# Kernel tuning notes

Measured on AMD Instinct MI355X. Metric: run time of the kernel, lower is better.

## Reference

```python
import jax, jax.numpy as jnp
import numpy as np

N = 100_000        # nodes
E = 800_000        # directed edges before symmetrization
IN_DIM = 18        # input_dim_wf + input_dim_vm
HID = 128
VM_NUM = 16        # each_vm_type_num * vm_types
B = 65536 // VM_NUM
NEG_SLOPE = 0.2    # PyG GATConv leaky_relu slope


def _gat_conv(h, src, dst, W, a_s, a_d, b, n):
    """PyG GATConv (heads=1, add_self_loops=True, dropout off)."""
    z = h @ W                                     # [n, C]
    loops = jnp.arange(n, dtype=src.dtype)
    s = jnp.concatenate([src, loops])
    d = jnp.concatenate([dst, loops])
    e_s = z @ a_s                                 # [n]
    e_d = z @ a_d
    alpha = jax.nn.leaky_relu(e_s[s] + e_d[d], NEG_SLOPE)   # [E']
    amax = jax.ops.segment_max(alpha, d, num_segments=n)    # stable softmax over incoming edges
    ex = jnp.exp(alpha - amax[d])
    denom = jax.ops.segment_sum(ex, d, num_segments=n)
    w = ex / denom[d]
    out = jax.ops.segment_sum(w[:, None] * z[s], d, num_segments=n)
    return out + b


def setup_inputs() -> dict:
    key = jax.random.key(0)
    ks = jax.random.split(key, 16)
    sc = 0.1
    inp = {
        'state_wf': jax.random.normal(ks[0], (N, IN_DIM), jnp.float32),
        'edge_index': jax.random.randint(ks[1], (2, E), 0, N, jnp.int32),
        'candidate_task_index': jax.random.randint(ks[2], (B * VM_NUM,), 0, N, jnp.int32),
        # GAT layer 0: 18 -> 128
        'W0': jax.random.normal(ks[3], (IN_DIM, HID), jnp.float32) * sc,
        'a_src0': jax.random.normal(ks[4], (HID,), jnp.float32) * sc,
        'a_dst0': jax.random.normal(ks[5], (HID,), jnp.float32) * sc,
        'b0': jnp.zeros((HID,), jnp.float32),
        # GAT layer 1: 128 -> 128
        'W1': jax.random.normal(ks[6], (HID, HID), jnp.float32) * sc,
        'a_src1': jax.random.normal(ks[7], (HID,), jnp.float32) * sc,
        'a_dst1': jax.random.normal(ks[8], (HID,), jnp.float32) * sc,
        'b1': jnp.zeros((HID,), jnp.float32),
        # actor MLP: Linear(128,128) + ReLU + Linear(128,1)
        'mW0': jax.random.normal(ks[9], (HID, HID), jnp.float32) * sc,
        'mb0': jnp.zeros((HID,), jnp.float32),
        'mW1': jax.random.normal(ks[10], (HID, 1), jnp.float32) * sc,
        'mb1': jnp.zeros((1,), jnp.float32),
    }
    return inp


def reference(state_wf, edge_index, candidate_task_index,
              W0, a_src0, a_dst0, b0, W1, a_src1, a_dst1, b1,
              mW0, mb0, mW1, mb1):
    # Actor.forward symmetrizes edges: cat(edge_index, edge_index.flip(0))
    src = jnp.concatenate([edge_index[0], edge_index[1]])
    dst = jnp.concatenate([edge_index[1], edge_index[0]])
    # GAT stack, F.elu after each conv (dropout=0)
    h = jax.nn.elu(_gat_conv(state_wf, src, dst, W0, a_src0, a_dst0, b0, N))
    h = jax.nn.elu(_gat_conv(h, src, dst, W1, a_src1, a_dst1, b1, N))
    # gather candidate tasks and score them
    cand = h[candidate_task_index].reshape(-1, VM_NUM, HID)       # [B, vm, H]
    scores = jax.nn.relu(cand @ mW0 + mb0) @ mW1 + mb1            # [B, vm, 1]
    pi = jax.nn.softmax(scores, axis=1)[..., 0]                   # softmax over dim=1
    return pi
```

## Files before the change

### kernel.cpp

```cpp
#include <hip/hip_runtime.h>
#include <hip/hip_bf16.h>
#include <math.h>
#include <stdint.h>

typedef __hip_bfloat16 bf16;
typedef __attribute__((ext_vector_type(8))) short s8v;
typedef __attribute__((ext_vector_type(4))) float f4v;

#define N_NODES 100000
#define HID 128
#define NEG 0.2f
#define NBUCK 256
#define BSHIFT 9
#define INDIM 18

__device__ __forceinline__ float b2f(bf16 x) { return __bfloat162float(x); }
__device__ __forceinline__ bf16 f2b(float x) { return __float2bfloat16(x); }
__device__ __forceinline__ float lo_bf(unsigned int u) {
    union { unsigned int i; float f; } c; c.i = u << 16; return c.f;
}
__device__ __forceinline__ float hi_bf(unsigned int u) {
    union { unsigned int i; float f; } c; c.i = u & 0xffff0000u; return c.f;
}
__device__ __forceinline__ short bfbits(float x) {
    union { bf16 b; short s; } u; u.b = f2b(x); return u.s;
}


__global__ void k_bhist(const int* __restrict__ ei, int E, int* __restrict__ bcnt) {
    __shared__ int h[NBUCK];
    int t = threadIdx.x;
    h[t] = 0;
    __syncthreads();
    int i = blockIdx.x * blockDim.x + t;
    int stride = gridDim.x * blockDim.x;
    for (; i < E; i += stride) {
        int u = ei[i], v = ei[E + i];
        atomicAdd(&h[v >> BSHIFT], 1);
        atomicAdd(&h[u >> BSHIFT], 1);
    }
    __syncthreads();
    if (h[t]) atomicAdd(&bcnt[t], h[t]);
}

__global__ void k_bscan(const int* __restrict__ bcnt, int* __restrict__ bbase,
                        int* __restrict__ bnext) {
    __shared__ int buf[2][NBUCK];
    int t = threadIdx.x;
    int v = bcnt[t];
    buf[0][t] = v;
    __syncthreads();
    int cur = 0;
    for (int off = 1; off < NBUCK; off <<= 1) {
        int x = buf[cur][t] + ((t >= off) ? buf[cur][t - off] : 0);
        buf[cur ^ 1][t] = x;
        cur ^= 1;
        __syncthreads();
    }
    int incl = buf[cur][t];
    int excl = incl - v;
    bbase[t] = excl;
    bnext[t] = excl;
    if (t == NBUCK - 1) bbase[NBUCK] = incl;
}

#define SCH 2048
#define SK 8
__global__ __launch_bounds__(256) void k_bscatter(const int* __restrict__ ei, int E,
                                                  int* __restrict__ bnext,
                                                  unsigned* __restrict__ pairs) {
    __shared__ int h[NBUCK], base[NBUCK], h2[NBUCK];
    int t = threadIdx.x;
    h[t] = 0; h2[t] = 0;
    __syncthreads();
    int b0 = blockIdx.x * SCH;
    int eu[SK], ev[SK];
#pragma unroll
    for (int k = 0; k < SK; k++) {
        int i = b0 + k * 256 + t;
        if (i < E) {
            int u = ei[i], v = ei[E + i];
            eu[k] = u; ev[k] = v;
            atomicAdd(&h[v >> BSHIFT], 1);
            atomicAdd(&h[u >> BSHIFT], 1);
        } else { eu[k] = -1; ev[k] = -1; }
    }
    __syncthreads();
    if (h[t] > 0) base[t] = atomicAdd(&bnext[t], h[t]);
    __syncthreads();
#pragma unroll
    for (int k = 0; k < SK; k++) {
        if (eu[k] >= 0) {
            unsigned u = (unsigned)eu[k], v = (unsigned)ev[k];
            int bv = v >> BSHIFT;
            pairs[base[bv] + atomicAdd(&h2[bv], 1)] = ((v & 511u) << 17) | u;
            int bu = u >> BSHIFT;
            pairs[base[bu] + atomicAdd(&h2[bu], 1)] = ((u & 511u) << 17) | v;
        }
    }
}

__global__ __launch_bounds__(256) void k_bbuild(const unsigned* __restrict__ pairs,
                                                const int* __restrict__ bbase,
                                                int* __restrict__ rowptr,
                                                int* __restrict__ col, int n) {
    __shared__ int deg[512];
    __shared__ int off[512];
    __shared__ int s2[2][256];
    int t = threadIdx.x;
    int b = blockIdx.x;
    int node0 = b << BSHIFT;
    deg[t] = 0; deg[t + 256] = 0;
    __syncthreads();
    int p0 = bbase[b], p1 = bbase[b + 1];
    for (int i = p0 + t; i < p1; i += 256) atomicAdd(&deg[pairs[i] >> 17], 1);
    __syncthreads();
    int a0 = deg[2 * t], a1 = deg[2 * t + 1];
    int s = a0 + a1;
    s2[0][t] = s;
    __syncthreads();
    int cur = 0;
    for (int o = 1; o < 256; o <<= 1) {
        int x = s2[cur][t] + ((t >= o) ? s2[cur][t - o] : 0);
        s2[cur ^ 1][t] = x;
        cur ^= 1;
        __syncthreads();
    }
    int excl = s2[cur][t] - s;
    off[2 * t] = excl;
    off[2 * t + 1] = excl + a0;
    __syncthreads();
    for (int j = t; j < 512; j += 256) {
        int node = node0 + j;
        if (node <= n) rowptr[node] = p0 + off[j];
    }
    deg[t] = 0; deg[t + 256] = 0;
    __syncthreads();
    for (int i = p0 + t; i < p1; i += 256) {
        unsigned pr = pairs[i];
        int d = pr >> 17;
        int ofs = atomicAdd(&deg[d], 1);
        col[p0 + off[d] + ofs] = (int)(pr & 0x1FFFFu);
    }
}


__device__ void pack128(const float* __restrict__ W, short* __restrict__ frag, int b) {
    int idx = b * 256 + threadIdx.x;
    int j = idx & 7;
    int lane = (idx >> 3) & 63;
    int cb = (idx >> 9) & 7;
    int kb = idx >> 12;
    int k = kb * 32 + (lane >> 4) * 8 + j;
    int c = cb * 16 + (lane & 15);
    float w = W[k * HID + c];
    bf16 hi = f2b(w);
    frag[idx] = bfbits(w);
    frag[16384 + idx] = bfbits(w - b2f(hi));
}

__global__ void k_packall(const float* __restrict__ W1, const float* __restrict__ mW0,
                          const float* __restrict__ W0, short* __restrict__ W1f,
                          short* __restrict__ mW0f, short* __restrict__ W0f) {
    int b = blockIdx.x;
    if (b < 64) { pack128(W1, W1f, b); return; }
    if (b < 128) { pack128(mW0, mW0f, b - 64); return; }
    int idx = (b - 128) * 256 + threadIdx.x;
    int var = idx >> 13;
    int r = idx & 8191;
    int j = r & 7;
    int lane = (r >> 3) & 63;
    int cb = (r >> 9) & 7;
    int kb = r >> 12;
    int kp = kb * 32 + (lane >> 4) * 8 + j;
    int c = cb * 16 + (lane & 15);
    short out = 0;
    if (kp < 2 * INDIM) {
        int src = (kp < INDIM) ? kp : kp - INDIM;
        float w = W0[src * HID + c];
        bf16 hi = f2b(w);
        bool want_hi = (kp < INDIM) ^ (var == 1);
        out = want_hi ? bfbits(w) : bfbits(w - b2f(hi));
    }
    W0f[var * 8192 + r] = out;
}


__global__ __launch_bounds__(256) void k_feat0m(const float* __restrict__ x,
                        const short* __restrict__ Wf,
                        const float* __restrict__ as_, const float* __restrict__ ad_,
                        bf16* __restrict__ z, float* __restrict__ es, float* __restrict__ ed,
                        int n) {
    __shared__ __align__(16) short ztile[4][16][136];
    int wv = threadIdx.x >> 6, lane = threadIdx.x & 63;
    int node0 = (blockIdx.x * 4 + wv) * 16;
    if (node0 >= n) return;
    int m = lane & 15, q = lane >> 4;
    const float* xr = x + (size_t)(node0 + m) * INDIM;
    s8v af0, af1;
#pragma unroll
    for (int j = 0; j < 8; j++) {
        int p0 = q * 8 + j;
        float v0 = 0.f;
        if (p0 < INDIM) v0 = xr[p0];
        else if (p0 < 2 * INDIM) v0 = xr[p0 - INDIM];
        short o0;
        if (p0 < INDIM) o0 = bfbits(v0);
        else o0 = bfbits(v0 - b2f(f2b(v0)));
        af0[j] = o0;
        int p1 = 32 + q * 8 + j;
        float v1 = (p1 < 2 * INDIM) ? xr[p1 - INDIM] : 0.f;
        af1[j] = bfbits(v1 - b2f(f2b(v1)));
    }
    f4v acc[8];
#pragma unroll
    for (int cb = 0; cb < 8; cb++) acc[cb] = (f4v){0.f, 0.f, 0.f, 0.f};
    const s8v* wf = (const s8v*)Wf;
#pragma unroll
    for (int cb = 0; cb < 8; cb++) {
        acc[cb] = __builtin_amdgcn_mfma_f32_16x16x32_bf16(af0, wf[cb * 64 + lane], acc[cb], 0, 0, 0);
        acc[cb] = __builtin_amdgcn_mfma_f32_16x16x32_bf16(af1, wf[(8 + cb) * 64 + lane], acc[cb], 0, 0, 0);
        acc[cb] = __builtin_amdgcn_mfma_f32_16x16x32_bf16(af0, wf[1024 + cb * 64 + lane], acc[cb], 0, 0, 0);
        acc[cb] = __builtin_amdgcn_mfma_f32_16x16x32_bf16(af1, wf[1024 + (8 + cb) * 64 + lane], acc[cb], 0, 0, 0);
    }
    float pe[4] = {0.f, 0.f, 0.f, 0.f}, pd[4] = {0.f, 0.f, 0.f, 0.f};
#pragma unroll
    for (int cb = 0; cb < 8; cb++) {
        float asv = as_[cb * 16 + m];
        float adv = ad_[cb * 16 + m];
#pragma unroll
        for (int r = 0; r < 4; r++) { pe[r] += acc[cb][r] * asv; pd[r] += acc[cb][r] * adv; }
    }
#pragma unroll
    for (int r = 0; r < 4; r++) {
#pragma unroll
        for (int off = 1; off < 16; off <<= 1) {
            pe[r] += __shfl_xor(pe[r], off);
            pd[r] += __shfl_xor(pd[r], off);
        }
    }
    if (m == 0) {
#pragma unroll
        for (int r = 0; r < 4; r++) {
            es[node0 + q * 4 + r] = pe[r];
            ed[node0 + q * 4 + r] = pd[r];
        }
    }
#pragma unroll
    for (int cb = 0; cb < 8; cb++)
#pragma unroll
        for (int r = 0; r < 4; r++)
            ztile[wv][q * 4 + r][cb * 16 + m] = bfbits(acc[cb][r]);
#pragma unroll
    for (int i = 0; i < 4; i++) {
        int idx = i * 64 + lane;
        int row = idx >> 4, t = idx & 15;
        s8v v = *(const s8v*)&ztile[wv][row][t * 8];
        *(s8v*)((short*)z + (size_t)(node0 + row) * HID + t * 8) = v;
    }
}


__global__ __launch_bounds__(256) void k_feat1(const bf16* __restrict__ h,
                        const short* __restrict__ Wf,
                        const float* __restrict__ as_, const float* __restrict__ ad_,
                        bf16* __restrict__ z, float* __restrict__ es, float* __restrict__ ed,
                        int n) {
    __shared__ __align__(16) short ztile[4][16][136];
    int wv = threadIdx.x >> 6, lane = threadIdx.x & 63;
    int node0 = (blockIdx.x * 4 + wv) * 16;
    if (node0 >= n) return;
    int m = lane & 15, q = lane >> 4;
    const short* hrow = (const short*)h + (size_t)(node0 + m) * HID + q * 8;
    s8v af[4];
#pragma unroll
    for (int kb = 0; kb < 4; kb++) af[kb] = *(const s8v*)(hrow + kb * 32);
    f4v acc[8];
#pragma unroll
    for (int cb = 0; cb < 8; cb++) acc[cb] = (f4v){0.f, 0.f, 0.f, 0.f};
    const s8v* wf = (const s8v*)Wf;
#pragma unroll
    for (int kb = 0; kb < 4; kb++) {
#pragma unroll
        for (int cb = 0; cb < 8; cb++) {
            acc[cb] = __builtin_amdgcn_mfma_f32_16x16x32_bf16(af[kb], wf[(kb * 8 + cb) * 64 + lane], acc[cb], 0, 0, 0);
            acc[cb] = __builtin_amdgcn_mfma_f32_16x16x32_bf16(af[kb], wf[2048 + (kb * 8 + cb) * 64 + lane], acc[cb], 0, 0, 0);
        }
    }
    float pe[4] = {0.f, 0.f, 0.f, 0.f}, pd[4] = {0.f, 0.f, 0.f, 0.f};
#pragma unroll
    for (int cb = 0; cb < 8; cb++) {
        float asv = as_[cb * 16 + m];
        float adv = ad_[cb * 16 + m];
#pragma unroll
        for (int r = 0; r < 4; r++) { pe[r] += acc[cb][r] * asv; pd[r] += acc[cb][r] * adv; }
    }
#pragma unroll
    for (int r = 0; r < 4; r++) {
#pragma unroll
        for (int off = 1; off < 16; off <<= 1) {
            pe[r] += __shfl_xor(pe[r], off);
            pd[r] += __shfl_xor(pd[r], off);
        }
    }
    if (m == 0) {
#pragma unroll
        for (int r = 0; r < 4; r++) {
            es[node0 + q * 4 + r] = pe[r];
            ed[node0 + q * 4 + r] = pd[r];
        }
    }
#pragma unroll
    for (int cb = 0; cb < 8; cb++)
#pragma unroll
        for (int r = 0; r < 4; r++)
            ztile[wv][q * 4 + r][cb * 16 + m] = bfbits(acc[cb][r]);
#pragma unroll
    for (int i = 0; i < 4; i++) {
        int idx = i * 64 + lane;
        int row = idx >> 4, t = idx & 15;
        s8v v = *(const s8v*)&ztile[wv][row][t * 8];
        *(s8v*)((short*)z + (size_t)(node0 + row) * HID + t * 8) = v;
    }
}


__global__ __launch_bounds__(256) void k_agg(const bf16* __restrict__ z,
                      const int* __restrict__ rowptr, const int* __restrict__ col,
                      const float* __restrict__ es, const float* __restrict__ ed,
                      const float* __restrict__ bias, bf16* __restrict__ hout, int n) {
    int wv = threadIdx.x >> 6;
    int lane = threadIdx.x & 63;
    int d = blockIdx.x * 4 + wv;
    if (d >= n) return;
    int s0 = rowptr[d], s1 = rowptr[d + 1];
    float edv = ed[d];
    int g = lane >> 4, t = lane & 15;
    const uint4* zr = (const uint4*)z;
    float acc[8];
#pragma unroll
    for (int j = 0; j < 8; j++) acc[j] = 0.f;
    float den = 0.f;
    for (int e0 = s0; e0 < s1; e0 += 8) {
        int eA = e0 + g, eB = e0 + 4 + g;
        bool okA = (eA < s1), okB = (eB < s1);
        int sA = col[okA ? eA : s1 - 1];
        int sB = col[okB ? eB : s1 - 1];
        float aA = es[sA] + edv; aA = aA > 0.f ? aA : NEG * aA;
        float aB = es[sB] + edv; aB = aB > 0.f ? aB : NEG * aB;
        float pA = okA ? __expf(fminf(aA, 15.f)) : 0.f;
        float pB = okB ? __expf(fminf(aB, 15.f)) : 0.f;
        uint4 rA = zr[(size_t)sA * 16 + t];
        uint4 rB = zr[(size_t)sB * 16 + t];
        den += pA + pB;
        acc[0] += pA * lo_bf(rA.x) + pB * lo_bf(rB.x);
        acc[1] += pA * hi_bf(rA.x) + pB * hi_bf(rB.x);
        acc[2] += pA * lo_bf(rA.y) + pB * lo_bf(rB.y);
        acc[3] += pA * hi_bf(rA.y) + pB * hi_bf(rB.y);
        acc[4] += pA * lo_bf(rA.z) + pB * lo_bf(rB.z);
        acc[5] += pA * hi_bf(rA.z) + pB * hi_bf(rB.z);
        acc[6] += pA * lo_bf(rA.w) + pB * lo_bf(rB.w);
        acc[7] += pA * hi_bf(rA.w) + pB * hi_bf(rB.w);
    }
#pragma unroll
    for (int off = 16; off <= 32; off <<= 1) {
        den += __shfl_xor(den, off);
#pragma unroll
        for (int j = 0; j < 8; j++) acc[j] += __shfl_xor(acc[j], off);
    }
    if (g == 0) {
        float aself = es[d] + edv;
        aself = aself > 0.f ? aself : NEG * aself;
        float pself = __expf(fminf(aself, 15.f));
        den += pself;
        uint4 raw = zr[(size_t)d * 16 + t];
        acc[0] += pself * lo_bf(raw.x); acc[1] += pself * hi_bf(raw.x);
        acc[2] += pself * lo_bf(raw.y); acc[3] += pself * hi_bf(raw.y);
        acc[4] += pself * lo_bf(raw.z); acc[5] += pself * hi_bf(raw.z);
        acc[6] += pself * lo_bf(raw.w); acc[7] += pself * hi_bf(raw.w);
        float inv = 1.f / den;
        union { bf16 hv[8]; uint4 v; } uo;
#pragma unroll
        for (int j = 0; j < 8; j++) {
            float o = acc[j] * inv + bias[t * 8 + j];
            o = o > 0.f ? o : (__expf(o) - 1.f);
            uo.hv[j] = f2b(o);
        }
        ((uint4*)hout)[(size_t)d * 16 + t] = uo.v;
    }
}


__global__ __launch_bounds__(256) void k_group(const bf16* __restrict__ h,
                        const int* __restrict__ cand,
                        const short* __restrict__ Wf, const float* __restrict__ mb0,
                        const float* __restrict__ mW1, const float* __restrict__ mb1,
                        float* __restrict__ out) {
    __shared__ float sc[4][16];
    int wv = threadIdx.x >> 6, lane = threadIdx.x & 63;
    int g = blockIdx.x * 4 + wv;
    int m = lane & 15, q = lane >> 4;
    int node = cand[g * 16 + m];
    const short* hrow = (const short*)h + (size_t)node * HID + q * 8;
    s8v af[4];
#pragma unroll
    for (int kb = 0; kb < 4; kb++) af[kb] = *(const s8v*)(hrow + kb * 32);
    f4v acc[8];
#pragma unroll
    for (int cb = 0; cb < 8; cb++) acc[cb] = (f4v){0.f, 0.f, 0.f, 0.f};
    const s8v* wf = (const s8v*)Wf;
#pragma unroll
    for (int kb = 0; kb < 4; kb++) {
#pragma unroll
        for (int cb = 0; cb < 8; cb++) {
            acc[cb] = __builtin_amdgcn_mfma_f32_16x16x32_bf16(af[kb], wf[(kb * 8 + cb) * 64 + lane], acc[cb], 0, 0, 0);
            acc[cb] = __builtin_amdgcn_mfma_f32_16x16x32_bf16(af[kb], wf[2048 + (kb * 8 + cb) * 64 + lane], acc[cb], 0, 0, 0);
        }
    }
    float sr[4] = {0.f, 0.f, 0.f, 0.f};
#pragma unroll
    for (int cb = 0; cb < 8; cb++) {
        float b0v = mb0[cb * 16 + m];
        float w1v = mW1[cb * 16 + m];
#pragma unroll
        for (int r = 0; r < 4; r++) sr[r] += fmaxf(acc[cb][r] + b0v, 0.f) * w1v;
    }
#pragma unroll
    for (int r = 0; r < 4; r++) {
#pragma unroll
        for (int off = 1; off < 16; off <<= 1) sr[r] += __shfl_xor(sr[r], off);
    }
    float b1v = mb1[0];
    if (m == 0) {
#pragma unroll
        for (int r = 0; r < 4; r++) sc[wv][q * 4 + r] = sr[r] + b1v;
    }
    if (lane < 16) {
        float s = sc[wv][lane];
        float mx = s;
#pragma unroll
        for (int off = 1; off < 16; off <<= 1) mx = fmaxf(mx, __shfl_xor(mx, off));
        float e = __expf(s - mx);
        float den = e;
#pragma unroll
        for (int off = 1; off < 16; off <<= 1) den += __shfl_xor(den, off);
        out[g * 16 + lane] = e / den;
    }
}


extern "C" void kernel_launch(void* const* d_in, const int* in_sizes, int n_in,
                              void* d_out, int out_size, void* d_ws, size_t ws_size,
                              hipStream_t stream) {
    const int N = N_NODES;
    const float* state = (const float*)d_in[0];
    const int* ei   = (const int*)d_in[1];
    const int* cand = (const int*)d_in[2];
    const float* W0  = (const float*)d_in[3];
    const float* as0 = (const float*)d_in[4];
    const float* ad0 = (const float*)d_in[5];
    const float* b0  = (const float*)d_in[6];
    const float* W1  = (const float*)d_in[7];
    const float* as1 = (const float*)d_in[8];
    const float* ad1 = (const float*)d_in[9];
    const float* b1  = (const float*)d_in[10];
    const float* mW0 = (const float*)d_in[11];
    const float* mb0 = (const float*)d_in[12];
    const float* mW1 = (const float*)d_in[13];
    const float* mb1 = (const float*)d_in[14];

    int E = in_sizes[1] / 2;
    int M = 2 * E;
    int ncand = in_sizes[2];
    int ngroups = ncand / 16;

    char* p = (char*)d_ws;
    bf16* zb = (bf16*)p;              p += (size_t)N * HID * 2;
    bf16* hb = (bf16*)p;              p += (size_t)N * HID * 2;
    float* es = (float*)p;            p += (size_t)N * 4;
    float* ed = (float*)p;            p += (size_t)N * 4;
    p = (char*)(((uintptr_t)p + 15) & ~(uintptr_t)15);
    short* W1frag  = (short*)p;       p += 32768 * 2;
    short* mW0frag = (short*)p;       p += 32768 * 2;
    short* W0frag  = (short*)p;       p += 16384 * 2;
    int* rowptr = (int*)p;            p += (size_t)(N + 1) * 4;
    int* col    = (int*)p;            p += (size_t)M * 4;
    int* bcnt   = (int*)p;            p += (NBUCK + 1) * 4;
    int* bbase  = (int*)p;            p += (NBUCK + 1) * 4;
    int* bnext  = (int*)p;            p += NBUCK * 4;
    unsigned* pairs = (unsigned*)zb;

    int nwb = N / 4;

    k_packall<<<192, 256, 0, stream>>>(W1, mW0, W0, W1frag, mW0frag, W0frag);

    hipMemsetAsync(bcnt, 0, NBUCK * sizeof(int), stream);
    k_bhist<<<512, 256, 0, stream>>>(ei, E, bcnt);
    k_bscan<<<1, NBUCK, 0, stream>>>(bcnt, bbase, bnext);
    k_bscatter<<<(E + SCH - 1) / SCH, 256, 0, stream>>>(ei, E, bnext, pairs);
    k_bbuild<<<NBUCK, 256, 0, stream>>>(pairs, bbase, rowptr, col, N);

    int nfb = (N / 16 + 3) / 4;
    k_feat0m<<<nfb, 256, 0, stream>>>(state, W0frag, as0, ad0, zb, es, ed, N);
    k_agg<<<nwb, 256, 0, stream>>>(zb, rowptr, col, es, ed, b0, hb, N);

    k_feat1<<<nfb, 256, 0, stream>>>(hb, W1frag, as1, ad1, zb, es, ed, N);
    k_agg<<<nwb, 256, 0, stream>>>(zb, rowptr, col, es, ed, b1, hb, N);

    k_group<<<ngroups / 4, 256, 0, stream>>>(hb, cand, mW0frag, mb0, mW1, mb1, (float*)d_out);
}
```

Before: 347.8 us.

## Fuse weight packing with histogram and edge scatter with layer-0 features

Merges the weight-packing kernel and the bucket histogram into one launch, with per-block partial histograms written to a buffer so the global memset and atomics go away. The scan then sums those partials. The edge scatter and the layer-0 feature transform now share one launch as heterogeneous blocks, which needs a dedicated pairs buffer instead of aliasing the z buffer. This cuts kernel launches and lets independent work overlap, at the cost of extra workspace memory and a serial partial sum in the single-block scan.

After: 326.2 us. 1.07x faster.

```diff
diff --git a/kernel.cpp b/kernel.cpp
--- a/kernel.cpp
+++ b/kernel.cpp
@@ -13,6 +13,7 @@
 #define NBUCK 256
 #define BSHIFT 9
 #define INDIM 18
+#define NHB 128
 
 __device__ __forceinline__ float b2f(bf16 x) { return __bfloat162float(x); }
 __device__ __forceinline__ bf16 f2b(float x) { return __float2bfloat16(x); }
@@ -24,124 +25,6 @@
 }
 __device__ __forceinline__ short bfbits(float x) {
     union { bf16 b; short s; } u; u.b = f2b(x); return u.s;
-}
-
-
-__global__ void k_bhist(const int* __restrict__ ei, int E, int* __restrict__ bcnt) {
-    __shared__ int h[NBUCK];
-    int t = threadIdx.x;
-    h[t] = 0;
-    __syncthreads();
-    int i = blockIdx.x * blockDim.x + t;
-    int stride = gridDim.x * blockDim.x;
-    for (; i < E; i += stride) {
-        int u = ei[i], v = ei[E + i];
-        atomicAdd(&h[v >> BSHIFT], 1);
-        atomicAdd(&h[u >> BSHIFT], 1);
-    }
-    __syncthreads();
-    if (h[t]) atomicAdd(&bcnt[t], h[t]);
-}
-
-__global__ void k_bscan(const int* __restrict__ bcnt, int* __restrict__ bbase,
-                        int* __restrict__ bnext) {
-    __shared__ int buf[2][NBUCK];
-    int t = threadIdx.x;
-    int v = bcnt[t];
-    buf[0][t] = v;
-    __syncthreads();
-    int cur = 0;
-    for (int off = 1; off < NBUCK; off <<= 1) {
-        int x = buf[cur][t] + ((t >= off) ? buf[cur][t - off] : 0);
-        buf[cur ^ 1][t] = x;
-        cur ^= 1;
-        __syncthreads();
-    }
-    int incl = buf[cur][t];
-    int excl = incl - v;
-    bbase[t] = excl;
-    bnext[t] = excl;
-    if (t == NBUCK - 1) bbase[NBUCK] = incl;
-}
-
-#define SCH 2048
-#define SK 8
-__global__ __launch_bounds__(256) void k_bscatter(const int* __restrict__ ei, int E,
-                                                  int* __restrict__ bnext,
-                                                  unsigned* __restrict__ pairs) {
-    __shared__ int h[NBUCK], base[NBUCK], h2[NBUCK];
-    int t = threadIdx.x;
-    h[t] = 0; h2[t] = 0;
-    __syncthreads();
-    int b0 = blockIdx.x * SCH;
-    int eu[SK], ev[SK];
-#pragma unroll
-    for (int k = 0; k < SK; k++) {
-        int i = b0 + k * 256 + t;
-        if (i < E) {
-            int u = ei[i], v = ei[E + i];
-            eu[k] = u; ev[k] = v;
-            atomicAdd(&h[v >> BSHIFT], 1);
-            atomicAdd(&h[u >> BSHIFT], 1);
-        } else { eu[k] = -1; ev[k] = -1; }
-    }
-    __syncthreads();
-    if (h[t] > 0) base[t] = atomicAdd(&bnext[t], h[t]);
-    __syncthreads();
-#pragma unroll
-    for (int k = 0; k < SK; k++) {
-        if (eu[k] >= 0) {
-            unsigned u = (unsigned)eu[k], v = (unsigned)ev[k];
-            int bv = v >> BSHIFT;
-            pairs[base[bv] + atomicAdd(&h2[bv], 1)] = ((v & 511u) << 17) | u;
-            int bu = u >> BSHIFT;
-            pairs[base[bu] + atomicAdd(&h2[bu], 1)] = ((u & 511u) << 17) | v;
-        }
-    }
-}
-
-__global__ __launch_bounds__(256) void k_bbuild(const unsigned* __restrict__ pairs,
-                                                const int* __restrict__ bbase,
-                                                int* __restrict__ rowptr,
-                                                int* __restrict__ col, int n) {
-    __shared__ int deg[512];
-    __shared__ int off[512];
-    __shared__ int s2[2][256];
-    int t = threadIdx.x;
-    int b = blockIdx.x;
-    int node0 = b << BSHIFT;
-    deg[t] = 0; deg[t + 256] = 0;
-    __syncthreads();
-    int p0 = bbase[b], p1 = bbase[b + 1];
-    for (int i = p0 + t; i < p1; i += 256) atomicAdd(&deg[pairs[i] >> 17], 1);
-    __syncthreads();
-    int a0 = deg[2 * t], a1 = deg[2 * t + 1];
-    int s = a0 + a1;
-    s2[0][t] = s;
-    __syncthreads();
-    int cur = 0;
-    for (int o = 1; o < 256; o <<= 1) {
-        int x = s2[cur][t] + ((t >= o) ? s2[cur][t - o] : 0);
-        s2[cur ^ 1][t] = x;
-        cur ^= 1;
-        __syncthreads();
-    }
-    int excl = s2[cur][t] - s;
-    off[2 * t] = excl;
-    off[2 * t + 1] = excl + a0;
-    __syncthreads();
-    for (int j = t; j < 512; j += 256) {
-        int node = node0 + j;
-        if (node <= n) rowptr[node] = p0 + off[j];
-    }
-    deg[t] = 0; deg[t + 256] = 0;
-    __syncthreads();
-    for (int i = p0 + t; i < p1; i += 256) {
-        unsigned pr = pairs[i];
-        int d = pr >> 17;
-        int ofs = atomicAdd(&deg[d], 1);
-        col[p0 + off[d] + ofs] = (int)(pr & 0x1FFFFu);
-    }
 }
 
 
@@ -159,41 +42,119 @@
     frag[16384 + idx] = bfbits(w - b2f(hi));
 }
 
-__global__ void k_packall(const float* __restrict__ W1, const float* __restrict__ mW0,
-                          const float* __restrict__ W0, short* __restrict__ W1f,
-                          short* __restrict__ mW0f, short* __restrict__ W0f) {
+__global__ __launch_bounds__(256) void k_prep(const float* __restrict__ W1,
+                          const float* __restrict__ mW0, const float* __restrict__ W0,
+                          short* __restrict__ W1f, short* __restrict__ mW0f,
+                          short* __restrict__ W0f,
+                          const int* __restrict__ ei, int E, int* __restrict__ part) {
     int b = blockIdx.x;
+    int t = threadIdx.x;
     if (b < 64) { pack128(W1, W1f, b); return; }
     if (b < 128) { pack128(mW0, mW0f, b - 64); return; }
-    int idx = (b - 128) * 256 + threadIdx.x;
-    int var = idx >> 13;
-    int r = idx & 8191;
-    int j = r & 7;
-    int lane = (r >> 3) & 63;
-    int cb = (r >> 9) & 7;
-    int kb = r >> 12;
-    int kp = kb * 32 + (lane >> 4) * 8 + j;
-    int c = cb * 16 + (lane & 15);
-    short out = 0;
-    if (kp < 2 * INDIM) {
-        int src = (kp < INDIM) ? kp : kp - INDIM;
-        float w = W0[src * HID + c];
-        bf16 hi = f2b(w);
-        bool want_hi = (kp < INDIM) ^ (var == 1);
-        out = want_hi ? bfbits(w) : bfbits(w - b2f(hi));
-    }
-    W0f[var * 8192 + r] = out;
-}
-
-
-__global__ __launch_bounds__(256) void k_feat0m(const float* __restrict__ x,
-                        const short* __restrict__ Wf,
+    if (b < 192) {
+        int idx = (b - 128) * 256 + t;
+        int var = idx >> 13;
+        int r = idx & 8191;
+        int j = r & 7;
+        int lane = (r >> 3) & 63;
+        int cb = (r >> 9) & 7;
+        int kb = r >> 12;
+        int kp = kb * 32 + (lane >> 4) * 8 + j;
+        int c = cb * 16 + (lane & 15);
+        short out = 0;
+        if (kp < 2 * INDIM) {
+            int src = (kp < INDIM) ? kp : kp - INDIM;
+            float w = W0[src * HID + c];
+            bf16 hi = f2b(w);
+            bool want_hi = (kp < INDIM) ^ (var == 1);
+            out = want_hi ? bfbits(w) : bfbits(w - b2f(hi));
+        }
+        W0f[var * 8192 + r] = out;
+        return;
+    }
+    __shared__ int h[NBUCK];
+    int hb = b - 192;
+    h[t] = 0;
+    __syncthreads();
+    int i = hb * 256 + t;
+    int stride = NHB * 256;
+    for (; i < E; i += stride) {
+        int u = ei[i], v = ei[E + i];
+        atomicAdd(&h[v >> BSHIFT], 1);
+        atomicAdd(&h[u >> BSHIFT], 1);
+    }
+    __syncthreads();
+    part[hb * NBUCK + t] = h[t];
+}
+
+
+__global__ void k_bscan(const int* __restrict__ part, int* __restrict__ bbase,
+                        int* __restrict__ bnext) {
+    __shared__ int buf[2][NBUCK];
+    int t = threadIdx.x;
+    int v = 0;
+    for (int b = 0; b < NHB; b++) v += part[b * NBUCK + t];
+    buf[0][t] = v;
+    __syncthreads();
+    int cur = 0;
+    for (int off = 1; off < NBUCK; off <<= 1) {
+        int x = buf[cur][t] + ((t >= off) ? buf[cur][t - off] : 0);
+        buf[cur ^ 1][t] = x;
+        cur ^= 1;
+        __syncthreads();
+    }
+    int incl = buf[cur][t];
+    int excl = incl - v;
+    bbase[t] = excl;
+    bnext[t] = excl;
+    if (t == NBUCK - 1) bbase[NBUCK] = incl;
+}
+
+
+#define SCH 2048
+#define SK 8
+__global__ __launch_bounds__(256) void k_scat_feat0(const int* __restrict__ ei, int E,
+                        int* __restrict__ bnext, unsigned* __restrict__ pairs, int nscat,
+                        const float* __restrict__ x, const short* __restrict__ Wf,
                         const float* __restrict__ as_, const float* __restrict__ ad_,
                         bf16* __restrict__ z, float* __restrict__ es, float* __restrict__ ed,
                         int n) {
+    __shared__ int h[NBUCK], base[NBUCK], h2[NBUCK];
     __shared__ __align__(16) short ztile[4][16][136];
+    if (blockIdx.x < (unsigned)nscat) {
+        int t = threadIdx.x;
+        h[t] = 0; h2[t] = 0;
+        __syncthreads();
+        int b0 = blockIdx.x * SCH;
+        int eu[SK], ev[SK];
+#pragma unroll
+        for (int k = 0; k < SK; k++) {
+            int i = b0 + k * 256 + t;
+            if (i < E) {
+                int u = ei[i], v = ei[E + i];
+                eu[k] = u; ev[k] = v;
+                atomicAdd(&h[v >> BSHIFT], 1);
+                atomicAdd(&h[u >> BSHIFT], 1);
+            } else { eu[k] = -1; ev[k] = -1; }
+        }
+        __syncthreads();
+        if (h[t] > 0) base[t] = atomicAdd(&bnext[t], h[t]);
+        __syncthreads();
+#pragma unroll
+        for (int k = 0; k < SK; k++) {
+            if (eu[k] >= 0) {
+                unsigned u = (unsigned)eu[k], v = (unsigned)ev[k];
+                int bv = v >> BSHIFT;
+                pairs[base[bv] + atomicAdd(&h2[bv], 1)] = ((v & 511u) << 17) | u;
+                int bu = u >> BSHIFT;
+                pairs[base[bu] + atomicAdd(&h2[bu], 1)] = ((u & 511u) << 17) | v;
+            }
+        }
+        return;
+    }
+    int fb = blockIdx.x - nscat;
     int wv = threadIdx.x >> 6, lane = threadIdx.x & 63;
-    int node0 = (blockIdx.x * 4 + wv) * 16;
+    int node0 = (fb * 4 + wv) * 16;
     if (node0 >= n) return;
     int m = lane & 15, q = lane >> 4;
     const float* xr = x + (size_t)(node0 + m) * INDIM;
@@ -257,6 +218,51 @@
         int row = idx >> 4, t = idx & 15;
         s8v v = *(const s8v*)&ztile[wv][row][t * 8];
         *(s8v*)((short*)z + (size_t)(node0 + row) * HID + t * 8) = v;
+    }
+}
+
+
+__global__ __launch_bounds__(256) void k_bbuild(const unsigned* __restrict__ pairs,
+                                                const int* __restrict__ bbase,
+                                                int* __restrict__ rowptr,
+                                                int* __restrict__ col, int n) {
+    __shared__ int deg[512];
+    __shared__ int off[512];
+    __shared__ int s2[2][256];
+    int t = threadIdx.x;
+    int b = blockIdx.x;
+    int node0 = b << BSHIFT;
+    deg[t] = 0; deg[t + 256] = 0;
+    __syncthreads();
+    int p0 = bbase[b], p1 = bbase[b + 1];
+    for (int i = p0 + t; i < p1; i += 256) atomicAdd(&deg[pairs[i] >> 17], 1);
+    __syncthreads();
+    int a0 = deg[2 * t], a1 = deg[2 * t + 1];
+    int s = a0 + a1;
+    s2[0][t] = s;
+    __syncthreads();
+    int cur = 0;
+    for (int o = 1; o < 256; o <<= 1) {
+        int x = s2[cur][t] + ((t >= o) ? s2[cur][t - o] : 0);
+        s2[cur ^ 1][t] = x;
+        cur ^= 1;
+        __syncthreads();
+    }
+    int excl = s2[cur][t] - s;
+    off[2 * t] = excl;
+    off[2 * t + 1] = excl + a0;
+    __syncthreads();
+    for (int j = t; j < 512; j += 256) {
+        int node = node0 + j;
+        if (node <= n) rowptr[node] = p0 + off[j];
+    }
+    deg[t] = 0; deg[t + 256] = 0;
+    __syncthreads();
+    for (int i = p0 + t; i < p1; i += 256) {
+        unsigned pr = pairs[i];
+        int d = pr >> 17;
+        int ofs = atomicAdd(&deg[d], 1);
+        col[p0 + off[d] + ofs] = (int)(pr & 0x1FFFFu);
     }
 }
 
@@ -485,27 +491,22 @@
     short* W0frag  = (short*)p;       p += 16384 * 2;
     int* rowptr = (int*)p;            p += (size_t)(N + 1) * 4;
     int* col    = (int*)p;            p += (size_t)M * 4;
-    int* bcnt   = (int*)p;            p += (NBUCK + 1) * 4;
+    unsigned* pairs = (unsigned*)p;   p += (size_t)M * 4;
+    int* part   = (int*)p;            p += NHB * NBUCK * 4;
     int* bbase  = (int*)p;            p += (NBUCK + 1) * 4;
     int* bnext  = (int*)p;            p += NBUCK * 4;
-    unsigned* pairs = (unsigned*)zb;
 
     int nwb = N / 4;
-
-    k_packall<<<192, 256, 0, stream>>>(W1, mW0, W0, W1frag, mW0frag, W0frag);
-
-    hipMemsetAsync(bcnt, 0, NBUCK * sizeof(int), stream);
-    k_bhist<<<512, 256, 0, stream>>>(ei, E, bcnt);
-    k_bscan<<<1, NBUCK, 0, stream>>>(bcnt, bbase, bnext);
-    k_bscatter<<<(E + SCH - 1) / SCH, 256, 0, stream>>>(ei, E, bnext, pairs);
+    int nfb = (N / 16 + 3) / 4;
+    int nscat = (E + SCH - 1) / SCH;
+
+    k_prep<<<192 + NHB, 256, 0, stream>>>(W1, mW0, W0, W1frag, mW0frag, W0frag, ei, E, part);
+    k_bscan<<<1, NBUCK, 0, stream>>>(part, bbase, bnext);
+    k_scat_feat0<<<nscat + nfb, 256, 0, stream>>>(ei, E, bnext, pairs, nscat,
+                                                  state, W0frag, as0, ad0, zb, es, ed, N);
     k_bbuild<<<NBUCK, 256, 0, stream>>>(pairs, bbase, rowptr, col, N);
-
-    int nfb = (N / 16 + 3) / 4;
-    k_feat0m<<<nfb, 256, 0, stream>>>(state, W0frag, as0, ad0, zb, es, ed, N);
     k_agg<<<nwb, 256, 0, stream>>>(zb, rowptr, col, es, ed, b0, hb, N);
-
     k_feat1<<<nfb, 256, 0, stream>>>(hb, W1frag, as1, ad1, zb, es, ed, N);
     k_agg<<<nwb, 256, 0, stream>>>(zb, rowptr, col, es, ed, b1, hb, N);
-
     k_group<<<ngroups / 4, 256, 0, stream>>>(hb, cand, mW0frag, mb0, mW1, mb1, (float*)d_out);
 }
```
